# Performance work log

Hardware: AMD Instinct MI355X
Metric: run time of the kernel (lower is better)

## Reference

```python
import jax, jax.numpy as jnp
import numpy as np

N_NODES = 200000
N_EDGES = 6400000
T = 6        # member feature dim
M = 10       # fingerprint dim
R = 3        # extra rounds (R+1 total linears)
G_IN = 14    # group feature dim
G_OUT = 4    # group perceptron output dim


def setup_inputs() -> dict:
    key = jax.random.key(0)
    ks = jax.random.split(key, 10)
    x_member = jax.random.normal(ks[0], (N_NODES, T), dtype=jnp.float32)
    x_group = jax.random.normal(ks[1], (1, G_IN), dtype=jnp.float32)
    edge_src = jax.random.randint(ks[2], (N_EDGES,), 0, N_NODES, dtype=jnp.int32)
    edge_dst = jax.random.randint(ks[3], (N_EDGES,), 0, N_NODES, dtype=jnp.int32)
    # learned parameters
    H0 = jax.random.normal(ks[4], (T, M), dtype=jnp.float32) / np.sqrt(T)   # round-0 linear
    Hs = jax.random.normal(ks[5], (R, M, M), dtype=jnp.float32) / np.sqrt(M)  # rounds 1..R
    Wsc = jnp.full((R + 1,), 0.2, dtype=jnp.float32)  # scalar W[L], init 0.2 as in source
    Wg = jax.random.normal(ks[6], (G_IN, G_OUT), dtype=jnp.float32) / np.sqrt(G_IN)
    Wm = jax.random.normal(ks[7], (M + G_OUT, 3), dtype=jnp.float32) / np.sqrt(M + G_OUT)
    return {"x_member": x_member, "x_group": x_group, "edge_src": edge_src,
            "edge_dst": edge_dst, "H0": H0, "Hs": Hs, "Wsc": Wsc, "Wg": Wg, "Wm": Wm}


def reference(x_member, x_group, edge_src, edge_dst, H0, Hs, Wsc, Wg, Wm):
    N = x_member.shape[0]
    # Round 0: neighbor sum in member-feature space (t=6), project to m=10.
    nbr0 = jax.ops.segment_sum(x_member[edge_src], edge_dst, num_segments=N)  # [N, t]
    r = jax.nn.sigmoid((x_member + nbr0) @ H0)                                # [N, m]
    # fingerprint f accumulates softmax(r * W_L) over all nodes and rounds
    f = jnp.sum(jax.nn.softmax(r * Wsc[0], axis=-1), axis=0, keepdims=True)   # [1, m]

    def step(carry, params):
        r, f = carry
        H, w = params
        nbr = jax.ops.segment_sum(r[edge_src], edge_dst, num_segments=N)      # [N, m]
        r = jax.nn.sigmoid((r + nbr) @ H)                                     # [N, m]
        f = f + jnp.sum(jax.nn.softmax(r * w, axis=-1), axis=0, keepdims=True)
        return (r, f), None

    (r, f), _ = jax.lax.scan(step, (r, f), (Hs, Wsc[1:]))
    group_out = x_group @ Wg                                                  # [1, g_out]
    merged = jnp.concatenate([f, group_out], axis=1) @ Wm                     # [1, 3]
    return merged
```

## Files before the change

### kernel.cpp

```cpp
#include <hip/hip_runtime.h>
#include <hip/hip_fp16.h>
#include <math.h>

#define N_NODES 200000
#define N_EDGES 6400000
#define T 6
#define M 10

#define NB    782
#define NBLK  256
#define CH    25000
#define GHLEN (NB * NBLK)
#define CAP   14336

#define SBLOCKS 196

#define PASSC_LDS_INTS  (CH + 4 * NB + 1024)
#define PASSC_LDS_BYTES (PASSC_LDS_INTS * 4)

#define LCAP 9216

typedef __attribute__((ext_vector_type(2))) float vf2;
typedef __attribute__((ext_vector_type(4))) unsigned int u32x4;

__global__ __launch_bounds__(256) void convert_kernel(
    const float* __restrict__ x, __half* __restrict__ xh)
{
    int i = blockIdx.x * 256 + threadIdx.x;
    if (i >= N_NODES) return;
    const vf2* p = (const vf2*)(x + (size_t)i * 6);
    vf2 a = __builtin_nontemporal_load(p);
    vf2 b = __builtin_nontemporal_load(p + 1);
    vf2 c = __builtin_nontemporal_load(p + 2);
    union { __half2 h[4]; u32x4 q; } u;
    u.h[0] = __floats2half2_rn(a.x, a.y);
    u.h[1] = __floats2half2_rn(b.x, b.y);
    u.h[2] = __floats2half2_rn(c.x, c.y);
    u.h[3] = __floats2half2_rn(0.f, 0.f);
    __builtin_nontemporal_store(u.q, (u32x4*)(xh + (size_t)i * 8));
}

__global__ __launch_bounds__(1024) void passA_kernel(
    const int* __restrict__ dst, int* __restrict__ gh)
{
    __shared__ int lh[NB];
    int g = blockIdx.x;
    for (int t = threadIdx.x; t < NB; t += 1024) lh[t] = 0;
    __syncthreads();
    int base = g * CH;
    int end  = base + CH; if (end > N_EDGES) end = N_EDGES;
    for (int e = base + threadIdx.x; e < end; e += 1024)
        atomicAdd(&lh[__builtin_nontemporal_load(dst + e) >> 8], 1);
    __syncthreads();
    for (int t = threadIdx.x; t < NB; t += 1024) gh[t * NBLK + g] = lh[t];
}

__global__ __launch_bounds__(1024) void scan1_kernel(
    int* __restrict__ gh, int* __restrict__ bsum)
{
    __shared__ int sbuf[1024];
    int tid = threadIdx.x;
    int t   = blockIdx.x * 1024 + tid;
    int v   = (t < GHLEN) ? gh[t] : 0;
    sbuf[tid] = v;
    __syncthreads();
    for (int d = 1; d < 1024; d <<= 1) {
        int u = (tid >= d) ? sbuf[tid - d] : 0;
        __syncthreads();
        sbuf[tid] += u;
        __syncthreads();
    }
    if (t < GHLEN) gh[t] = sbuf[tid] - v;
    if (tid == 1023) bsum[blockIdx.x] = sbuf[1023];
}

__global__ __launch_bounds__(256) void scan2_kernel(int* __restrict__ bsum)
{
    __shared__ int sbuf[256];
    int tid = threadIdx.x;
    int v = (tid < SBLOCKS) ? bsum[tid] : 0;
    sbuf[tid] = v;
    __syncthreads();
    for (int d = 1; d < 256; d <<= 1) {
        int u = (tid >= d) ? sbuf[tid - d] : 0;
        __syncthreads();
        sbuf[tid] += u;
        __syncthreads();
    }
    if (tid < SBLOCKS) bsum[tid] = sbuf[tid] - v;
}

__global__ __launch_bounds__(1024) void scan3_kernel(
    int* __restrict__ gh, const int* __restrict__ bsum)
{
    int t = blockIdx.x * 1024 + threadIdx.x;
    if (t < GHLEN) gh[t] += bsum[blockIdx.x];
}

__global__ __launch_bounds__(1024) void passC_kernel(
    const int* __restrict__ src, const int* __restrict__ dst,
    const int* __restrict__ gh, int* __restrict__ ebuf)
{
    extern __shared__ int dyn[];
    int* earr = dyn;
    int* cnt  = dyn + CH;
    int* ls   = cnt + NB;
    int* lcur = ls + NB;
    int* gs   = lcur + NB;
    int* sbuf = gs + NB;

    int g   = blockIdx.x;
    int tid = threadIdx.x;

    for (int b = tid; b < NB; b += 1024) {
        int idx = b * NBLK + g;
        int s0  = gh[idx];
        int s1  = (idx + 1 < GHLEN) ? gh[idx + 1] : N_EDGES;
        gs[b]  = s0;
        cnt[b] = s1 - s0;
    }
    __syncthreads();

    int v = (tid < NB) ? cnt[tid] : 0;
    sbuf[tid] = v;
    __syncthreads();
    for (int d = 1; d < 1024; d <<= 1) {
        int u = (tid >= d) ? sbuf[tid - d] : 0;
        __syncthreads();
        sbuf[tid] += u;
        __syncthreads();
    }
    if (tid < NB) { int e0 = sbuf[tid] - v; ls[tid] = e0; lcur[tid] = e0; }
    __syncthreads();

    int base = g * CH;
    for (int e = base + tid; e < base + CH; e += 1024) {
        int s = __builtin_nontemporal_load(src + e);
        int d = __builtin_nontemporal_load(dst + e);
        int b = d >> 8;
        int p = atomicAdd(&lcur[b], 1);
        earr[p] = (s << 8) | (d & 255);
    }
    __syncthreads();

    int wv = tid >> 6, lane = tid & 63;
    for (int b = wv; b < NB; b += 16) {
        int bl = ls[b], bg = gs[b], c = cnt[b];
        for (int o = lane; o < c; o += 64)
            ebuf[bg + o] = earr[bl + o];
    }
}

__global__ __launch_bounds__(256) void passD_kernel(
    const int* __restrict__ gh, int* __restrict__ col, int* __restrict__ off)
{
    __shared__ int earr[CAP];
    __shared__ int hist[256];
    __shared__ int incl[256];
    int b = blockIdx.x;
    int ebase = gh[b * NBLK];
    int eend  = (b == NB - 1) ? N_EDGES : gh[(b + 1) * NBLK];
    int n = eend - ebase;
    if (n > CAP) n = CAP;
    for (int k = threadIdx.x; k < n; k += 256)
        earr[k] = __builtin_nontemporal_load(col + ebase + k);
    hist[threadIdx.x] = 0;
    __syncthreads();
    for (int k = threadIdx.x; k < n; k += 256) atomicAdd(&hist[earr[k] & 255], 1);
    __syncthreads();
    int t = threadIdx.x;
    int h = hist[t];
    incl[t] = h;
    __syncthreads();
    for (int d = 1; d < 256; d <<= 1) {
        int v = (t >= d) ? incl[t - d] : 0;
        __syncthreads();
        incl[t] += v;
        __syncthreads();
    }
    int node = b * 256 + t;
    if (node < N_NODES) off[node] = ebase + incl[t];
    hist[t] = incl[t] - h;
    __syncthreads();
    for (int k = threadIdx.x; k < n; k += 256) {
        int e = earr[k];
        int p = atomicAdd(&hist[e & 255], 1);
        col[ebase + p] = e >> 8;
    }
}

template<int TD, bool FP8IN>
__device__ inline void accum_row(u32x4 q, float* v)
{
    if (FP8IN) {
        vf2 f0 = __builtin_amdgcn_cvt_pk_f32_fp8(q.x, false);
        vf2 f1 = __builtin_amdgcn_cvt_pk_f32_fp8(q.x, true);
        vf2 f2 = __builtin_amdgcn_cvt_pk_f32_fp8(q.y, false);
        vf2 f3 = __builtin_amdgcn_cvt_pk_f32_fp8(q.y, true);
        vf2 f4 = __builtin_amdgcn_cvt_pk_f32_fp8(q.z, false);
        v[0] += f0.x; v[1] += f0.y; v[2] += f1.x; v[3] += f1.y;
        v[4] += f2.x; v[5] += f2.y; v[6] += f3.x; v[7] += f3.y;
        v[8] += f4.x; v[9] += f4.y;
    } else {
        union { u32x4 q; __half2 h[8]; } u; u.q = q;
#pragma unroll
        for (int k = 0; k < TD / 2; ++k) {
            float2 f = __half22float2(u.h[k]);
            v[2 * k] += f.x; v[2 * k + 1] += f.y;
        }
    }
}

template<int TD, bool FP8IN>
__global__ __launch_bounds__(256) void round_kernel(
    const u32x4* __restrict__ in,
    const int*   __restrict__ off,
    const int*   __restrict__ col,
    u32x4*       __restrict__ rout,
    const float* __restrict__ H,
    const float* __restrict__ Wsc, int widx,
    float*       __restrict__ facc)
{
    __shared__ int   lcol[LCAP];
    __shared__ int   shb[2];
    __shared__ float lsm[4][M];

    int b   = blockIdx.x;
    int tid = threadIdx.x;
    int i   = b * 256 + tid;

    if (tid == 0) {
        shb[0] = (b == 0) ? 0 : __builtin_nontemporal_load(off + b * 256 - 1);
        int lastnode = (b * 256 + 256 <= N_NODES) ? (b * 256 + 255) : (N_NODES - 1);
        shb[1] = __builtin_nontemporal_load(off + lastnode);
    }
    __syncthreads();
    int ebase  = shb[0];
    int nseg   = shb[1] - ebase;
    int nstage = nseg < LCAP ? nseg : LCAP;
    for (int k = tid; k < nstage; k += 256)
        lcol[k] = __builtin_nontemporal_load(col + ebase + k);
    __syncthreads();

    float w = Wsc[widx];
    float sm[M];

    if (i < N_NODES) {
        float v[TD];
#pragma unroll
        for (int t = 0; t < TD; ++t) v[t] = 0.0f;
        accum_row<TD, FP8IN>(in[i], v);
        int gstart = (i == 0) ? 0 : __builtin_nontemporal_load(off + i - 1);
        int gend   = __builtin_nontemporal_load(off + i);
        int js = gstart - ebase;
        int je = gend   - ebase;

        if (je <= nstage) {
            int j = js;
            for (; j + 8 <= je; j += 8) {
                int s0 = lcol[j];
                int s1 = lcol[j + 1];
                int s2 = lcol[j + 2];
                int s3 = lcol[j + 3];
                int s4 = lcol[j + 4];
                int s5 = lcol[j + 5];
                int s6 = lcol[j + 6];
                int s7 = lcol[j + 7];
                u32x4 q0 = in[s0], q1 = in[s1], q2 = in[s2], q3 = in[s3];
                u32x4 q4 = in[s4], q5 = in[s5], q6 = in[s6], q7 = in[s7];
                accum_row<TD, FP8IN>(q0, v);
                accum_row<TD, FP8IN>(q1, v);
                accum_row<TD, FP8IN>(q2, v);
                accum_row<TD, FP8IN>(q3, v);
                accum_row<TD, FP8IN>(q4, v);
                accum_row<TD, FP8IN>(q5, v);
                accum_row<TD, FP8IN>(q6, v);
                accum_row<TD, FP8IN>(q7, v);
            }
            for (; j < je; ++j)
                accum_row<TD, FP8IN>(in[lcol[j]], v);
        } else {
            for (int j = gstart; j < gend; ++j)
                accum_row<TD, FP8IN>(in[__builtin_nontemporal_load(col + j)], v);
        }

        float z[M];
#pragma unroll
        for (int m = 0; m < M; ++m) {
            float acc = 0.0f;
#pragma unroll
            for (int t = 0; t < TD; ++t) acc += v[t] * H[t * M + m];
            z[m] = acc;
        }
        float rr[M];
        float ssum = 0.0f;
#pragma unroll
        for (int m = 0; m < M; ++m) {
            rr[m] = 1.0f / (1.0f + __expf(-z[m]));
            sm[m] = __expf(rr[m] * w);
            ssum += sm[m];
        }
        {
            int d0 = __builtin_amdgcn_cvt_pk_fp8_f32(rr[0], rr[1], 0, false);
            d0     = __builtin_amdgcn_cvt_pk_fp8_f32(rr[2], rr[3], d0, true);
            int d1 = __builtin_amdgcn_cvt_pk_fp8_f32(rr[4], rr[5], 0, false);
            d1     = __builtin_amdgcn_cvt_pk_fp8_f32(rr[6], rr[7], d1, true);
            int d2 = __builtin_amdgcn_cvt_pk_fp8_f32(rr[8], rr[9], 0, false);
            u32x4 o = { (unsigned)d0, (unsigned)d1, (unsigned)d2, 0u };
            __builtin_nontemporal_store(o, rout + i);
        }
        float inv = 1.0f / ssum;
#pragma unroll
        for (int m = 0; m < M; ++m) sm[m] *= inv;
    } else {
#pragma unroll
        for (int m = 0; m < M; ++m) sm[m] = 0.0f;
    }

#pragma unroll
    for (int m = 0; m < M; ++m) {
        float x = sm[m];
#pragma unroll
        for (int o = 32; o > 0; o >>= 1) x += __shfl_down(x, o);
        sm[m] = x;
    }
    int lane = threadIdx.x & 63;
    int wv   = threadIdx.x >> 6;
    if (lane == 0) {
#pragma unroll
        for (int m = 0; m < M; ++m) lsm[wv][m] = sm[m];
    }
    __syncthreads();
    if (threadIdx.x < M) {
        float a = lsm[0][threadIdx.x] + lsm[1][threadIdx.x]
                + lsm[2][threadIdx.x] + lsm[3][threadIdx.x];
        atomicAdd(&facc[threadIdx.x], a);
    }
}

__global__ void final_kernel(const float* __restrict__ facc,
                             const float* __restrict__ xg,
                             const float* __restrict__ Wg,
                             const float* __restrict__ Wm,
                             float* __restrict__ out)
{
    if (threadIdx.x == 0 && blockIdx.x == 0) {
        float go[4];
        for (int g = 0; g < 4; ++g) {
            float a = 0.0f;
            for (int i = 0; i < 14; ++i) a += xg[i] * Wg[i * 4 + g];
            go[g] = a;
        }
        for (int j = 0; j < 3; ++j) {
            float o = 0.0f;
            for (int k = 0; k < M; ++k) o += facc[k] * Wm[k * 3 + j];
            for (int g = 0; g < 4; ++g)  o += go[g] * Wm[(M + g) * 3 + j];
            out[j] = o;
        }
    }
}

extern "C" void kernel_launch(void* const* d_in, const int* in_sizes, int n_in,
                              void* d_out, int out_size, void* d_ws, size_t ws_size,
                              hipStream_t stream)
{
    const float* x_member = (const float*)d_in[0];
    const float* x_group  = (const float*)d_in[1];
    const int*   edge_src = (const int*)  d_in[2];
    const int*   edge_dst = (const int*)  d_in[3];
    const float* H0       = (const float*)d_in[4];
    const float* Hs       = (const float*)d_in[5];
    const float* Wsc      = (const float*)d_in[6];
    const float* Wg       = (const float*)d_in[7];
    const float* Wm       = (const float*)d_in[8];
    float* out = (float*)d_out;

    char* w = (char*)d_ws;
    int*    col  = (int*)w;
    int*    off  = (int*)(w + 25600000);
    __half* xh   = (__half*)(w + 26400000);
    u32x4*  r0b  = (u32x4*)(w + 29600000);
    u32x4*  r1b  = (u32x4*)(w + 32800000);
    int*    gh   = (int*)(w + 32800000);
    int*    bsum = gh + GHLEN;
    float*  facc = (float*)(w + 36000000);

    static bool attr_done = false;
    if (!attr_done) {
        (void)hipFuncSetAttribute((const void*)passC_kernel,
                                  hipFuncAttributeMaxDynamicSharedMemorySize,
                                  PASSC_LDS_BYTES);
        attr_done = true;
    }

    (void)hipMemsetAsync(facc, 0, 64, stream);

    const int nblocks = (N_NODES + 255) / 256;

    convert_kernel<<<nblocks, 256, 0, stream>>>(x_member, xh);
    passA_kernel<<<NBLK, 1024, 0, stream>>>(edge_dst, gh);
    scan1_kernel<<<SBLOCKS, 1024, 0, stream>>>(gh, bsum);
    scan2_kernel<<<1, 256, 0, stream>>>(bsum);
    scan3_kernel<<<SBLOCKS, 1024, 0, stream>>>(gh, bsum);
    passC_kernel<<<NBLK, 1024, PASSC_LDS_BYTES, stream>>>(edge_src, edge_dst, gh, col);
    passD_kernel<<<NB, 256, 0, stream>>>(gh, col, off);

    round_kernel<T, false><<<nblocks, 256, 0, stream>>>((const u32x4*)xh, off, col, r0b, H0,             Wsc, 0, facc);
    round_kernel<M, true ><<<nblocks, 256, 0, stream>>>(r0b,              off, col, r1b, Hs + 0 * M * M, Wsc, 1, facc);
    round_kernel<M, true ><<<nblocks, 256, 0, stream>>>(r1b,              off, col, r0b, Hs + 1 * M * M, Wsc, 2, facc);
    round_kernel<M, true ><<<nblocks, 256, 0, stream>>>(r0b,              off, col, r1b, Hs + 2 * M * M, Wsc, 3, facc);

    final_kernel<<<1, 64, 0, stream>>>(facc, x_group, Wg, Wm, out);
}
```

Baseline: 396.7 us.

## Split each node's neighbor gather across two threads and widen passD blocks

The round kernels now launch 512 threads per block, with two threads per node. Each thread gathers half of the node's CSR neighbor list, and the partial sums are combined through an LDS buffer before the linear/sigmoid/softmax step. passD also moves to 512 threads so its load, histogram and scatter loops run with twice the threads. The aim is more memory-level parallelism in the latency-bound gathers (about 32 edges per node). The cost is an extra block barrier, more LDS per block, and half the threads sitting idle during the epilogue.

```diff
diff --git a/kernel.cpp b/kernel.cpp
--- a/kernel.cpp
+++ b/kernel.cpp
@@ -19,6 +19,7 @@
 #define PASSC_LDS_BYTES (PASSC_LDS_INTS * 4)
 
 #define LCAP 9216
+#define VSTRIDE 11
 
 typedef __attribute__((ext_vector_type(2))) float vf2;
 typedef __attribute__((ext_vector_type(4))) unsigned int u32x4;
@@ -151,38 +152,41 @@
     }
 }
 
-__global__ __launch_bounds__(256) void passD_kernel(
+__global__ __launch_bounds__(512) void passD_kernel(
     const int* __restrict__ gh, int* __restrict__ col, int* __restrict__ off)
 {
     __shared__ int earr[CAP];
     __shared__ int hist[256];
     __shared__ int incl[256];
-    int b = blockIdx.x;
+    int b   = blockIdx.x;
+    int tid = threadIdx.x;
     int ebase = gh[b * NBLK];
     int eend  = (b == NB - 1) ? N_EDGES : gh[(b + 1) * NBLK];
     int n = eend - ebase;
     if (n > CAP) n = CAP;
-    for (int k = threadIdx.x; k < n; k += 256)
+    for (int k = tid; k < n; k += 512)
         earr[k] = __builtin_nontemporal_load(col + ebase + k);
-    hist[threadIdx.x] = 0;
-    __syncthreads();
-    for (int k = threadIdx.x; k < n; k += 256) atomicAdd(&hist[earr[k] & 255], 1);
-    __syncthreads();
-    int t = threadIdx.x;
-    int h = hist[t];
-    incl[t] = h;
+    if (tid < 256) hist[tid] = 0;
+    __syncthreads();
+    for (int k = tid; k < n; k += 512) atomicAdd(&hist[earr[k] & 255], 1);
+    __syncthreads();
+    int t = tid;
+    int h = 0;
+    if (t < 256) { h = hist[t]; incl[t] = h; }
     __syncthreads();
     for (int d = 1; d < 256; d <<= 1) {
-        int v = (t >= d) ? incl[t - d] : 0;
-        __syncthreads();
-        incl[t] += v;
-        __syncthreads();
-    }
-    int node = b * 256 + t;
-    if (node < N_NODES) off[node] = ebase + incl[t];
-    hist[t] = incl[t] - h;
-    __syncthreads();
-    for (int k = threadIdx.x; k < n; k += 256) {
+        int v = (t < 256 && t >= d) ? incl[t - d] : 0;
+        __syncthreads();
+        if (t < 256) incl[t] += v;
+        __syncthreads();
+    }
+    if (t < 256) {
+        int node = b * 256 + t;
+        if (node < N_NODES) off[node] = ebase + incl[t];
+        hist[t] = incl[t] - h;
+    }
+    __syncthreads();
+    for (int k = tid; k < n; k += 512) {
         int e = earr[k];
         int p = atomicAdd(&hist[e & 255], 1);
         col[ebase + p] = e >> 8;
@@ -212,7 +216,7 @@
 }
 
 template<int TD, bool FP8IN>
-__global__ __launch_bounds__(256) void round_kernel(
+__global__ __launch_bounds__(512) void round_kernel(
     const u32x4* __restrict__ in,
     const int*   __restrict__ off,
     const int*   __restrict__ col,
@@ -223,11 +227,14 @@
 {
     __shared__ int   lcol[LCAP];
     __shared__ int   shb[2];
-    __shared__ float lsm[4][M];
-
-    int b   = blockIdx.x;
-    int tid = threadIdx.x;
-    int i   = b * 256 + tid;
+    __shared__ float vpart[256][VSTRIDE];
+    __shared__ float lsm[8][M];
+
+    int b    = blockIdx.x;
+    int tid  = threadIdx.x;
+    int nid  = tid & 255;
+    int half = tid >> 8;
+    int i    = b * 256 + nid;
 
     if (tid == 0) {
         shb[0] = (b == 0) ? 0 : __builtin_nontemporal_load(off + b * 256 - 1);
@@ -238,26 +245,32 @@
     int ebase  = shb[0];
     int nseg   = shb[1] - ebase;
     int nstage = nseg < LCAP ? nseg : LCAP;
-    for (int k = tid; k < nstage; k += 256)
+    for (int k = tid; k < nstage; k += 512)
         lcol[k] = __builtin_nontemporal_load(col + ebase + k);
     __syncthreads();
 
     float w = Wsc[widx];
     float sm[M];
-
-    if (i < N_NODES) {
-        float v[TD];
-#pragma unroll
-        for (int t = 0; t < TD; ++t) v[t] = 0.0f;
-        accum_row<TD, FP8IN>(in[i], v);
+    bool have = (i < N_NODES);
+
+    float v[TD];
+#pragma unroll
+    for (int t = 0; t < TD; ++t) v[t] = 0.0f;
+
+    if (have) {
         int gstart = (i == 0) ? 0 : __builtin_nontemporal_load(off + i - 1);
         int gend   = __builtin_nontemporal_load(off + i);
         int js = gstart - ebase;
         int je = gend   - ebase;
+        int jm = js + ((je - js + 1) >> 1);
+        int j0 = half ? jm : js;
+        int j1 = half ? je : jm;
+
+        if (half == 0) accum_row<TD, FP8IN>(in[i], v);
 
         if (je <= nstage) {
-            int j = js;
-            for (; j + 8 <= je; j += 8) {
+            int j = j0;
+            for (; j + 8 <= j1; j += 8) {
                 int s0 = lcol[j];
                 int s1 = lcol[j + 1];
                 int s2 = lcol[j + 2];
@@ -277,12 +290,23 @@
                 accum_row<TD, FP8IN>(q6, v);
                 accum_row<TD, FP8IN>(q7, v);
             }
-            for (; j < je; ++j)
+            for (; j < j1; ++j)
                 accum_row<TD, FP8IN>(in[lcol[j]], v);
         } else {
-            for (int j = gstart; j < gend; ++j)
-                accum_row<TD, FP8IN>(in[__builtin_nontemporal_load(col + j)], v);
-        }
+            for (int j = j0; j < j1; ++j)
+                accum_row<TD, FP8IN>(in[__builtin_nontemporal_load(col + ebase + j)], v);
+        }
+    }
+
+    if (half == 1) {
+#pragma unroll
+        for (int t = 0; t < TD; ++t) vpart[nid][t] = v[t];
+    }
+    __syncthreads();
+
+    if (have && half == 0) {
+#pragma unroll
+        for (int t = 0; t < TD; ++t) v[t] += vpart[nid][t];
 
         float z[M];
 #pragma unroll
@@ -324,17 +348,18 @@
         for (int o = 32; o > 0; o >>= 1) x += __shfl_down(x, o);
         sm[m] = x;
     }
-    int lane = threadIdx.x & 63;
-    int wv   = threadIdx.x >> 6;
+    int lane = tid & 63;
+    int wv   = tid >> 6;
     if (lane == 0) {
 #pragma unroll
         for (int m = 0; m < M; ++m) lsm[wv][m] = sm[m];
     }
     __syncthreads();
-    if (threadIdx.x < M) {
-        float a = lsm[0][threadIdx.x] + lsm[1][threadIdx.x]
-                + lsm[2][threadIdx.x] + lsm[3][threadIdx.x];
-        atomicAdd(&facc[threadIdx.x], a);
+    if (tid < M) {
+        float a = 0.0f;
+#pragma unroll
+        for (int k = 0; k < 8; ++k) a += lsm[k][tid];
+        atomicAdd(&facc[tid], a);
     }
 }
 
@@ -403,12 +428,12 @@
     scan2_kernel<<<1, 256, 0, stream>>>(bsum);
     scan3_kernel<<<SBLOCKS, 1024, 0, stream>>>(gh, bsum);
     passC_kernel<<<NBLK, 1024, PASSC_LDS_BYTES, stream>>>(edge_src, edge_dst, gh, col);
-    passD_kernel<<<NB, 256, 0, stream>>>(gh, col, off);
-
-    round_kernel<T, false><<<nblocks, 256, 0, stream>>>((const u32x4*)xh, off, col, r0b, H0,             Wsc, 0, facc);
-    round_kernel<M, true ><<<nblocks, 256, 0, stream>>>(r0b,              off, col, r1b, Hs + 0 * M * M, Wsc, 1, facc);
-    round_kernel<M, true ><<<nblocks, 256, 0, stream>>>(r1b,              off, col, r0b, Hs + 1 * M * M, Wsc, 2, facc);
-    round_kernel<M, true ><<<nblocks, 256, 0, stream>>>(r0b,              off, col, r1b, Hs + 2 * M * M, Wsc, 3, facc);
+    passD_kernel<<<NB, 512, 0, stream>>>(gh, col, off);
+
+    round_kernel<T, false><<<nblocks, 512, 0, stream>>>((const u32x4*)xh, off, col, r0b, H0,             Wsc, 0, facc);
+    round_kernel<M, true ><<<nblocks, 512, 0, stream>>>(r0b,              off, col, r1b, Hs + 0 * M * M, Wsc, 1, facc);
+    round_kernel<M, true ><<<nblocks, 512, 0, stream>>>(r1b,              off, col, r0b, Hs + 1 * M * M, Wsc, 2, facc);
+    round_kernel<M, true ><<<nblocks, 512, 0, stream>>>(r0b,              off, col, r1b, Hs + 2 * M * M, Wsc, 3, facc);
 
     final_kernel<<<1, 64, 0, stream>>>(facc, x_group, Wg, Wm, out);
 }
```

Result: no change. 403.5 us (+1.7%).
